# Kernel optimization log

Hardware: AMD Instinct MI355X
Metric: run time of the kernel (lower is better)

Reference implementation:

```python
import jax, jax.numpy as jnp
import numpy as np

T, B, D, K = 256, 128, 1024, 21
PAD = 0


def setup_inputs() -> dict:
    key = jax.random.key(0)
    k1, k2, k3, k4, k5, k6, k7 = jax.random.split(key, 7)
    lstm_features = jax.random.normal(k1, (T, B, D), dtype=jnp.float32)
    # gold tags: non-pad (1..K-1) for a random prefix, PAD afterwards; mask[0] all on
    tags = jax.random.randint(k2, (T, B), 1, K)
    lengths = jax.random.randint(k3, (B,), T // 2, T + 1)
    tags = jnp.where(jnp.arange(T)[:, None] < lengths[None, :], tags, PAD)
    W = jax.random.normal(k4, (D, K), dtype=jnp.float32) * 0.02
    b = jnp.zeros((K,), dtype=jnp.float32)
    # torchcrf initializes transitions uniform(-0.1, 0.1)
    start_transitions = jax.random.uniform(k5, (K,), minval=-0.1, maxval=0.1)
    end_transitions = jax.random.uniform(k6, (K,), minval=-0.1, maxval=0.1)
    transitions = jax.random.uniform(k7, (K, K), minval=-0.1, maxval=0.1)
    return {
        'lstm_features': lstm_features,
        'tags': tags,
        'W': W,
        'b': b,
        'start_transitions': start_transitions,
        'end_transitions': end_transitions,
        'transitions': transitions,
    }


def _crf_nll(emissions, tags, mask, start, end, trans):
    # emissions: (T,B,K), tags/mask: (T,B). Returns -sum_b log p(tags|emissions)
    maskf = mask.astype(emissions.dtype)
    # --- numerator: score of gold path (fully vectorized over t) ---
    em_score = jnp.take_along_axis(emissions, tags[:, :, None], axis=2)[:, :, 0]  # (T,B)
    tr_score = trans[tags[:-1], tags[1:]]                                          # (T-1,B)
    num = start[tags[0]] + em_score[0]
    num = num + jnp.sum((tr_score + em_score[1:]) * maskf[1:], axis=0)
    seq_ends = jnp.sum(mask.astype(jnp.int32), axis=0) - 1                         # (B,)
    last_tags = jnp.take_along_axis(tags, seq_ends[None, :], axis=0)[0]
    num = num + end[last_tags]
    # --- denominator: forward algorithm (log partition) via scan ---
    def step(score, xs):  # score: (B,K)
        emit_t, mask_t = xs
        nxt = jax.nn.logsumexp(score[:, :, None] + trans[None, :, :] + emit_t[:, None, :], axis=1)
        return jnp.where(mask_t[:, None], nxt, score), None
    score0 = start[None, :] + emissions[0]
    scoreT, _ = jax.lax.scan(step, score0, (emissions[1:], mask[1:]))
    den = jax.nn.logsumexp(scoreT + end[None, :], axis=1)                          # (B,)
    return -jnp.sum(num - den)


def _viterbi(emissions, mask, start, end, trans):
    # returns best tag sequence (T,B) int32, padded positions set to PAD
    n_tags = emissions.shape[-1]
    ident = jnp.arange(n_tags, dtype=jnp.int32)[None, :]
    def step(score, xs):  # score: (B,K)
        emit_t, mask_t = xs
        cand = score[:, :, None] + trans[None, :, :]          # (B, prev K, next K)
        best_prev = jnp.argmax(cand, axis=1).astype(jnp.int32)  # (B,K)
        nxt = jnp.max(cand, axis=1) + emit_t
        ptr = jnp.where(mask_t[:, None], best_prev, ident)    # identity ptr on padding
        new_score = jnp.where(mask_t[:, None], nxt, score)
        return new_score, ptr
    score0 = start[None, :] + emissions[0]
    scoreT, history = jax.lax.scan(step, score0, (emissions[1:], mask[1:]))  # history: (T-1,B,K)
    last_tag = jnp.argmax(scoreT + end[None, :], axis=1).astype(jnp.int32)   # (B,)
    def back(tag, hist_t):
        prev = jnp.take_along_axis(hist_t, tag[:, None], axis=1)[:, 0]
        return prev, tag
    first_tag, rest = jax.lax.scan(back, last_tag, history, reverse=True)    # rest = tags[1:]
    best = jnp.concatenate([first_tag[None, :], rest], axis=0)               # (T,B)
    return jnp.where(mask, best, PAD)


def reference(lstm_features, tags, W, b, start_transitions, end_transitions, transitions):
    # Linear projection; dropout is identity at inference
    fc_out = jnp.einsum('tbd,dk->tbk', lstm_features, W) + b
    mask = tags != PAD
    crf_out = _viterbi(fc_out, mask, start_transitions, end_transitions, transitions)
    crf_loss = _crf_nll(fc_out, tags, mask, start_transitions, end_transitions, transitions)
    return crf_out, crf_loss
```

## Files before the change

kernel.cpp:

```cpp
#include <hip/hip_runtime.h>
#include <math.h>

#define T_ 256
#define B_ 128
#define D_ 1024
#define K_ 21
#define NB3 43

typedef short v8s __attribute__((ext_vector_type(8)));
typedef float v4f __attribute__((ext_vector_type(4)));

__device__ __forceinline__ short bf16rne(float f) {
  unsigned u = __float_as_uint(f);
  u += 0x7FFFu + ((u >> 16) & 1u);
  return (short)(u >> 16);
}
__device__ __forceinline__ float rdl(float v, int l) {
  return __int_as_float(__builtin_amdgcn_readlane(__float_as_int(v), l));
}
__device__ __forceinline__ int imax3(int a, int b, int c) {
  const int t = a > b ? a : b;
  return t > c ? t : c;
}

typedef const __attribute__((address_space(1))) void* gas1_t;
typedef __attribute__((address_space(3))) void* las3_t;
__device__ __forceinline__ void gload_lds(const float* g, float* l) {
  __builtin_amdgcn_global_load_lds((gas1_t)g, (las3_t)l, 4, 0, 0);
}

__global__ __launch_bounds__(256) void fc_kernel(
    const float* __restrict__ A, const float* __restrict__ W,
    const float* __restrict__ bias, float* __restrict__ fc,
    float* __restrict__ out_loss) {
  __shared__ float red[3][64][22];
  if (blockIdx.x == 0 && threadIdx.x == 0) *out_loss = 0.f;
  const int lane = threadIdx.x & 63;
  const int wv = threadIdx.x >> 6;
  const int m15 = lane & 15, g4 = lane >> 4;
  const int rowbase = blockIdx.x * 64;
  const int kc = wv * 256;
  const int n1 = 16 + m15;

  v8s bf[8][2];
#pragma unroll
  for (int s = 0; s < 8; ++s) {
    const float* Wp = W + (size_t)(kc + 32 * s + 8 * g4) * K_;
#pragma unroll
    for (int j = 0; j < 8; ++j) bf[s][0][j] = bf16rne(Wp[j * K_ + m15]);
    if (n1 < K_) {
#pragma unroll
      for (int j = 0; j < 8; ++j) bf[s][1][j] = bf16rne(Wp[j * K_ + n1]);
    } else {
#pragma unroll
      for (int j = 0; j < 8; ++j) bf[s][1][j] = 0;
    }
  }

  v4f acc[4][2];
#pragma unroll
  for (int m = 0; m < 4; ++m) {
    acc[m][0] = (v4f)(0.f);
    acc[m][1] = (v4f)(0.f);
  }

#pragma unroll
  for (int s = 0; s < 8; ++s) {
    v8s av[4];
#pragma unroll
    for (int m = 0; m < 4; ++m) {
      const float* Ap =
          A + (size_t)(rowbase + 16 * m + m15) * D_ + kc + 32 * s + 8 * g4;
      const float4 x = *(const float4*)Ap;
      const float4 y = *(const float4*)(Ap + 4);
      av[m][0] = bf16rne(x.x); av[m][1] = bf16rne(x.y);
      av[m][2] = bf16rne(x.z); av[m][3] = bf16rne(x.w);
      av[m][4] = bf16rne(y.x); av[m][5] = bf16rne(y.y);
      av[m][6] = bf16rne(y.z); av[m][7] = bf16rne(y.w);
    }
#pragma unroll
    for (int m = 0; m < 4; ++m) {
      acc[m][0] = __builtin_amdgcn_mfma_f32_16x16x32_bf16(av[m], bf[s][0],
                                                          acc[m][0], 0, 0, 0);
      acc[m][1] = __builtin_amdgcn_mfma_f32_16x16x32_bf16(av[m], bf[s][1],
                                                          acc[m][1], 0, 0, 0);
    }
  }

  if (wv > 0) {
#pragma unroll
    for (int m = 0; m < 4; ++m)
#pragma unroll
      for (int ri = 0; ri < 4; ++ri) {
        const int rl = 16 * m + 4 * g4 + ri;
        red[wv - 1][rl][m15] = acc[m][0][ri];
        if (n1 < K_) red[wv - 1][rl][n1] = acc[m][1][ri];
      }
  }
  __syncthreads();
  if (wv == 0) {
    const float b0 = bias[m15];
    const float b1 = (n1 < K_) ? bias[n1] : 0.f;
#pragma unroll
    for (int m = 0; m < 4; ++m)
#pragma unroll
      for (int ri = 0; ri < 4; ++ri) {
        const int rl = 16 * m + 4 * g4 + ri;
        float* o = fc + (size_t)(rowbase + rl) * K_;
        o[m15] = acc[m][0][ri] + red[0][rl][m15] + red[1][rl][m15] +
                 red[2][rl][m15] + b0;
        if (n1 < K_)
          o[n1] = acc[m][1][ri] + red[0][rl][n1] + red[1][rl][n1] +
                  red[2][rl][n1] + b1;
      }
  }
}

__global__ __launch_bounds__(64) void scan_kernel(
    const float* __restrict__ fc, const int* __restrict__ tags,
    const float* __restrict__ startT, const float* __restrict__ endT,
    const float* __restrict__ trans, float* __restrict__ out_tags,
    float* __restrict__ out_loss) {
  __shared__ v4f statev[18];
  __shared__ float fcs[2][32][64];
  __shared__ unsigned short bp[256 * 66];
  __shared__ unsigned char h2[127 * 66];
  __shared__ unsigned char h4[63 * 66];
  __shared__ unsigned char cur[3 * 256];

  const int lane = threadIdx.x;
  const int blk = blockIdx.x;

  if (blk < 2 * NB3) {
    const bool fwd = blk < NB3;
    const int bblk = fwd ? blk : blk - NB3;
    int g = lane / 21;
    if (g > 2) g = 2;
    int jloc = lane - g * 21;
    if (jloc > 20) jloc = 20;
    const int gj = g * 21 + jloc;
    const int b0 = bblk * 3;

    int len0 = 0, len1 = 0, len2 = 0;
#pragma unroll
    for (int q = 0; q < 4; ++q) {
      const int t = q * 64 + lane;
      int bb0 = b0, bb1 = b0 + 1, bb2 = b0 + 2;
      if (bb1 >= B_) bb1 = B_ - 1;
      if (bb2 >= B_) bb2 = B_ - 1;
      len0 += __popcll(__ballot(tags[t * B_ + bb0] != 0));
      len1 += __popcll(__ballot(tags[t * B_ + bb1] != 0));
      len2 += __popcll(__ballot(tags[t * B_ + bb2] != 0));
    }
    const int mylen = (g == 0) ? len0 : (g == 1) ? len1 : len2;

    float* sb = (float*)statev + g * 24;
    const v4f* sv = (const v4f*)sb;

#define STAGE(c)                                                             \
    {                                                                        \
      const float* src_ = fc + ((size_t)((c) * 32) * B_ + b0) * K_ + lane;   \
      float* dst_ = &fcs[(c) & 1][0][0];                                     \
      _Pragma("unroll")                                                      \
      for (int q_ = 0; q_ < 32; ++q_)                                        \
        gload_lds(src_ + (size_t)q_ * (B_ * K_), dst_ + q_ * 64);            \
    }
#define WAIT_VM0()                                                           \
    {                                                                        \
      asm volatile("s_waitcnt vmcnt(0)" ::: "memory");                       \
      __builtin_amdgcn_sched_barrier(0);                                     \
    }

    STAGE(0)
    WAIT_VM0()
    const float em0 = fcs[0][0][gj];
    STAGE(1)

    if (fwd) {
      float ec[21];
#pragma unroll
      for (int i = 0; i < K_; ++i) ec[i] = __expf(trans[i * K_ + jloc]);
      float p = __expf(startT[jloc] + em0);
      sb[jloc] = p;
      float L = 0.f;

      for (int c = 0; c < 8; ++c) {
        const float* fb = &fcs[c & 1][0][0];
        const int t1 = c * 32 + 32;
        for (int t = c ? c * 32 : 1; t < t1; ++t) {
          const float emt = fb[(t & 31) * 64 + gj];
          const v4f A0 = sv[0], A1 = sv[1], A2 = sv[2], A3 = sv[3],
                    A4 = sv[4];
          const float A5 = sb[20];

          float d0 = A0[0] * ec[0], d1 = A0[1] * ec[1], d2 = A0[2] * ec[2];
          d0 = fmaf(A0[3], ec[3], d0); d1 = fmaf(A1[0], ec[4], d1);
          d2 = fmaf(A1[1], ec[5], d2);
          d0 = fmaf(A1[2], ec[6], d0); d1 = fmaf(A1[3], ec[7], d1);
          d2 = fmaf(A2[0], ec[8], d2);
          d0 = fmaf(A2[1], ec[9], d0); d1 = fmaf(A2[2], ec[10], d1);
          d2 = fmaf(A2[3], ec[11], d2);
          d0 = fmaf(A3[0], ec[12], d0); d1 = fmaf(A3[1], ec[13], d1);
          d2 = fmaf(A3[2], ec[14], d2);
          d0 = fmaf(A3[3], ec[15], d0); d1 = fmaf(A4[0], ec[16], d1);
          d2 = fmaf(A4[1], ec[17], d2);
          d0 = fmaf(A4[2], ec[18], d0); d1 = fmaf(A4[3], ec[19], d1);
          d2 = fmaf(A5, ec[20], d2);

          const float pn = ((d0 + d1) + d2) * __expf(emt);
          p = (t < mylen) ? pn : p;
          if ((t & 7) == 0) {
            const float f = A0[0];
            p *= __builtin_amdgcn_rcpf(f);
            L += __logf(f);
          }
          sb[jloc] = p;
        }
        if (c < 7) {
          WAIT_VM0()
          if (c + 2 < 8) STAGE(c + 2)
        }
      }

      const float w = p * __expf(endT[jloc]);
      float res = 0.f;
#pragma unroll
      for (int gg = 0; gg < 3; ++gg) {
        if (b0 + gg < B_) {
          float tot = 0.f;
#pragma unroll
          for (int i = 0; i < K_; ++i) tot += rdl(w, gg * K_ + i);
          res += rdl(L, gg * K_) + __logf(tot);
        }
      }
      if (lane == 0) atomicAdd(out_loss, res);
    } else {
      float tr[21];
#pragma unroll
      for (int i = 0; i < K_; ++i) tr[i] = trans[i * K_ + jloc] + 2048.0f;
      float sc = startT[jloc] + em0;
      sb[jloc] = sc;

      for (int c = 0; c < 8; ++c) {
        const float* fb = &fcs[c & 1][0][0];
        const int t1 = c * 32 + 32;
        for (int t = c ? c * 32 : 1; t < t1; ++t) {
          const float emt = fb[(t & 31) * 64 + gj];
          const v4f A0 = sv[0], A1 = sv[1], A2 = sv[2], A3 = sv[3],
                    A4 = sv[4];
          const float A5 = sb[20];

#define KEY(i, V) ((__float_as_int((V) + tr[i]) & 0xFFFFFFE0) | (20 - (i)))
          const int q0 = imax3(KEY(0, A0[0]), KEY(1, A0[1]), KEY(2, A0[2]));
          const int q1 = imax3(KEY(3, A0[3]), KEY(4, A1[0]), KEY(5, A1[1]));
          const int q2 = imax3(KEY(6, A1[2]), KEY(7, A1[3]), KEY(8, A2[0]));
          const int q3 = imax3(KEY(9, A2[1]), KEY(10, A2[2]), KEY(11, A2[3]));
          const int q4 = imax3(KEY(12, A3[0]), KEY(13, A3[1]), KEY(14, A3[2]));
          const int q5 = imax3(KEY(15, A3[3]), KEY(16, A4[0]), KEY(17, A4[1]));
          const int q6 = imax3(KEY(18, A4[2]), KEY(19, A4[3]), KEY(20, A5));
          const int km = imax3(imax3(q0, q1, q2), imax3(q3, q4, q5), q6);
#undef KEY
          const float nxt = __int_as_float(km & 0xFFFFFFE0) - 2048.0f + emt;
          const bool m = t < mylen;
          sc = m ? nxt : sc;
          sb[jloc] = sc;
          const int pw = m ? (20 - (km & 31)) : jloc;
          bp[t * 66 + g * 22 + jloc] = (unsigned short)pw;
        }
        if (c < 7) {
          WAIT_VM0()
          if (c + 2 < 8) STAGE(c + 2)
        }
      }
      __syncthreads();

      const float finb = sc + endT[jloc] + 2048.0f;
      const int myk = (__float_as_int(finb) & 0xFFFFFFE0) | (20 - jloc);
      int last0 = 0, last1 = 0, last2 = 0;
#pragma unroll
      for (int gg = 0; gg < 3; ++gg) {
        int km = 0;
#pragma unroll
        for (int i = 0; i < K_; ++i) {
          const int ki = __builtin_amdgcn_readlane(myk, gg * K_ + i);
          km = km > ki ? km : ki;
        }
        const int lt = 20 - (km & 31);
        if (gg == 0) last0 = lt;
        else if (gg == 1) last1 = lt;
        else last2 = lt;
      }

      for (int i = lane; i < 127 * 63; i += 64) {
        const int v = i / 63;
        const int rem = i - v * 63;
        const int gg = rem / 21, j = rem - (rem / 21) * 21;
        h2[v * 66 + gg * 22 + j] = (unsigned char)
            bp[(2 * v + 1) * 66 + gg * 22 + bp[(2 * v + 2) * 66 + gg * 22 + j]];
      }
      __syncthreads();
      for (int i = lane; i < 63 * 63; i += 64) {
        const int w = i / 63;
        const int rem = i - w * 63;
        const int gg = rem / 21, j = rem - (rem / 21) * 21;
        h4[w * 66 + gg * 22 + j] =
            h2[(2 * w) * 66 + gg * 22 + h2[(2 * w + 1) * 66 + gg * 22 + j]];
      }
      __syncthreads();

      if (lane < 3 && b0 + lane < B_) {
        int c = (lane == 0) ? last0 : (lane == 1) ? last1 : last2;
        cur[lane * 256 + 255] = (unsigned char)c;
        c = bp[255 * 66 + lane * 22 + c];
        cur[lane * 256 + 254] = (unsigned char)c;
        c = h2[126 * 66 + lane * 22 + c];
        cur[lane * 256 + 252] = (unsigned char)c;
        for (int w = 62; w >= 0; --w) {
          c = h4[w * 66 + lane * 22 + c];
          cur[lane * 256 + 4 * w] = (unsigned char)c;
        }
      }
      __syncthreads();
      for (int i = lane; i < 63 * 3; i += 64) {
        const int gg = i / 63, ii = i - (i / 63) * 63;
        const int t = 2 + 4 * ii;
        cur[gg * 256 + t] =
            h2[(t >> 1) * 66 + gg * 22 + cur[gg * 256 + t + 2]];
      }
      __syncthreads();
      for (int i = lane; i < 127 * 3; i += 64) {
        const int gg = i / 127, ii = i - (i / 127) * 127;
        const int t = 1 + 2 * ii;
        cur[gg * 256 + t] = (unsigned char)
            bp[(t + 1) * 66 + gg * 22 + cur[gg * 256 + t + 1]];
      }
      __syncthreads();
      for (int i = lane; i < 3 * 256; i += 64) {
        const int gg = i >> 8, t = i & 255;
        const int bb = b0 + gg;
        const int lg = (gg == 0) ? len0 : (gg == 1) ? len1 : len2;
        if (bb < B_)
          out_tags[t * B_ + bb] = (t < lg) ? (float)cur[gg * 256 + t] : 0.f;
      }
    }
#undef STAGE
#undef WAIT_VM0
  } else {
    const int b = blk - 2 * NB3;
    float contrib = 0.f;
#pragma unroll
    for (int q = 0; q < 4; ++q) {
      const int t = lane * 4 + q;
      const int tg = tags[t * B_ + b];
      const size_t ro = ((size_t)t * B_ + b) * K_;
      if (t == 0) {
        contrib += startT[tg] + fc[ro + tg];
      } else if (tg != 0) {
        const int pg = tags[(t - 1) * B_ + b];
        contrib += trans[pg * K_ + tg] + fc[ro + tg];
      }
      const bool isLast =
          (tg != 0) && (t == T_ - 1 || tags[(t + 1) * B_ + b] == 0);
      if (isLast) contrib += endT[tg];
    }
#pragma unroll
    for (int off = 32; off > 0; off >>= 1)
      contrib += __shfl_down(contrib, off, 64);
    if (lane == 0) atomicAdd(out_loss, -contrib);
  }
}

extern "C" void kernel_launch(void* const* d_in, const int* in_sizes, int n_in,
                              void* d_out, int out_size, void* d_ws,
                              size_t ws_size, hipStream_t stream) {
  const float* A = (const float*)d_in[0];
  const int* tags = (const int*)d_in[1];
  const float* W = (const float*)d_in[2];
  const float* bias = (const float*)d_in[3];
  const float* startT = (const float*)d_in[4];
  const float* endT = (const float*)d_in[5];
  const float* trans = (const float*)d_in[6];

  float* out_tags = (float*)d_out;
  float* out_loss = (float*)d_out + (size_t)T_ * B_;
  float* fc = (float*)d_ws;

  fc_kernel<<<512, 256, 0, stream>>>(A, W, bias, fc, out_loss);
  scan_kernel<<<2 * NB3 + B_, 64, 0, stream>>>(fc, tags, startT, endT, trans,
                                               out_tags, out_loss);
}
```

Before: 280.8 us.

## Process six sequences per scan block with two interleaved recurrence chains

Each forward/Viterbi scan block now handles six batch sequences instead of three. Every lane carries two independent recurrence chains (A and B) whose LDS loads and arithmetic are interleaved, so the work per step can overlap the latency of the serial dependency. This halves the number of scan blocks and doubles the LDS footprint and the backtracking work per block. Because the scan was already spread over many mostly idle CUs, the benefit depends on whether the extra instruction-level parallelism outweighs the longer per-step compute on the critical path.

```diff
diff --git a/kernel.cpp b/kernel.cpp
--- a/kernel.cpp
+++ b/kernel.cpp
@@ -5,7 +5,7 @@
 #define B_ 128
 #define D_ 1024
 #define K_ 21
-#define NB3 43
+#define NB6 22
 
 typedef short v8s __attribute__((ext_vector_type(8)));
 typedef float v4f __attribute__((ext_vector_type(4)));
@@ -121,49 +121,59 @@
     const float* __restrict__ startT, const float* __restrict__ endT,
     const float* __restrict__ trans, float* __restrict__ out_tags,
     float* __restrict__ out_loss) {
-  __shared__ v4f statev[18];
-  __shared__ float fcs[2][32][64];
-  __shared__ unsigned short bp[256 * 66];
-  __shared__ unsigned char h2[127 * 66];
-  __shared__ unsigned char h4[63 * 66];
-  __shared__ unsigned char cur[3 * 256];
+  __shared__ v4f statev[36];
+  __shared__ float fcs[2][32][128];
+  __shared__ unsigned short bp[256 * 132];
+  __shared__ unsigned char h2[127 * 132];
+  __shared__ unsigned char h4[63 * 132];
+  __shared__ unsigned char cur[6 * 256];
 
   const int lane = threadIdx.x;
   const int blk = blockIdx.x;
 
-  if (blk < 2 * NB3) {
-    const bool fwd = blk < NB3;
-    const int bblk = fwd ? blk : blk - NB3;
+  if (blk < 2 * NB6) {
+    const bool fwd = blk < NB6;
+    const int bblk = fwd ? blk : blk - NB6;
     int g = lane / 21;
     if (g > 2) g = 2;
     int jloc = lane - g * 21;
     if (jloc > 20) jloc = 20;
-    const int gj = g * 21 + jloc;
-    const int b0 = bblk * 3;
-
-    int len0 = 0, len1 = 0, len2 = 0;
+    const int gjA = g * 21 + jloc;
+    const int gjB = gjA + 63;
+    const int b0 = bblk * 6;
+
+    int len[6];
+#pragma unroll
+    for (int k = 0; k < 6; ++k) len[k] = 0;
 #pragma unroll
     for (int q = 0; q < 4; ++q) {
       const int t = q * 64 + lane;
-      int bb0 = b0, bb1 = b0 + 1, bb2 = b0 + 2;
-      if (bb1 >= B_) bb1 = B_ - 1;
-      if (bb2 >= B_) bb2 = B_ - 1;
-      len0 += __popcll(__ballot(tags[t * B_ + bb0] != 0));
-      len1 += __popcll(__ballot(tags[t * B_ + bb1] != 0));
-      len2 += __popcll(__ballot(tags[t * B_ + bb2] != 0));
-    }
-    const int mylen = (g == 0) ? len0 : (g == 1) ? len1 : len2;
-
-    float* sb = (float*)statev + g * 24;
-    const v4f* sv = (const v4f*)sb;
+#pragma unroll
+      for (int k = 0; k < 6; ++k) {
+        int bb = b0 + k;
+        if (bb >= B_) bb = B_ - 1;
+        len[k] += __popcll(__ballot(tags[t * B_ + bb] != 0));
+      }
+    }
+    const int len0 = len[0], len1 = len[1], len2 = len[2];
+    const int len3 = len[3], len4 = len[4], len5 = len[5];
+    const int mylenA = (g == 0) ? len0 : (g == 1) ? len1 : len2;
+    const int mylenB = (g == 0) ? len3 : (g == 1) ? len4 : len5;
+
+    float* sbA = (float*)statev + g * 24;
+    float* sbB = (float*)statev + (3 + g) * 24;
+    const v4f* svA = (const v4f*)sbA;
+    const v4f* svB = (const v4f*)sbB;
 
 #define STAGE(c)                                                             \
     {                                                                        \
       const float* src_ = fc + ((size_t)((c) * 32) * B_ + b0) * K_ + lane;   \
       float* dst_ = &fcs[(c) & 1][0][0];                                     \
       _Pragma("unroll")                                                      \
-      for (int q_ = 0; q_ < 32; ++q_)                                        \
-        gload_lds(src_ + (size_t)q_ * (B_ * K_), dst_ + q_ * 64);            \
+      for (int q_ = 0; q_ < 32; ++q_) {                                      \
+        gload_lds(src_ + (size_t)q_ * (B_ * K_), dst_ + q_ * 128);           \
+        gload_lds(src_ + (size_t)q_ * (B_ * K_) + 64, dst_ + q_ * 128 + 64); \
+      }                                                                      \
     }
 #define WAIT_VM0()                                                           \
     {                                                                        \
@@ -173,48 +183,75 @@
 
     STAGE(0)
     WAIT_VM0()
-    const float em0 = fcs[0][0][gj];
+    const float em0A = fcs[0][0][gjA];
+    const float em0B = fcs[0][0][gjB];
     STAGE(1)
+
+    const float st0 = startT[jloc];
 
     if (fwd) {
       float ec[21];
 #pragma unroll
       for (int i = 0; i < K_; ++i) ec[i] = __expf(trans[i * K_ + jloc]);
-      float p = __expf(startT[jloc] + em0);
-      sb[jloc] = p;
-      float L = 0.f;
+      float pA = __expf(st0 + em0A), pB = __expf(st0 + em0B);
+      float LA = 0.f, LB = 0.f;
+      sbA[jloc] = pA;
+      sbB[jloc] = pB;
 
       for (int c = 0; c < 8; ++c) {
         const float* fb = &fcs[c & 1][0][0];
         const int t1 = c * 32 + 32;
         for (int t = c ? c * 32 : 1; t < t1; ++t) {
-          const float emt = fb[(t & 31) * 64 + gj];
-          const v4f A0 = sv[0], A1 = sv[1], A2 = sv[2], A3 = sv[3],
-                    A4 = sv[4];
-          const float A5 = sb[20];
-
-          float d0 = A0[0] * ec[0], d1 = A0[1] * ec[1], d2 = A0[2] * ec[2];
-          d0 = fmaf(A0[3], ec[3], d0); d1 = fmaf(A1[0], ec[4], d1);
-          d2 = fmaf(A1[1], ec[5], d2);
-          d0 = fmaf(A1[2], ec[6], d0); d1 = fmaf(A1[3], ec[7], d1);
-          d2 = fmaf(A2[0], ec[8], d2);
-          d0 = fmaf(A2[1], ec[9], d0); d1 = fmaf(A2[2], ec[10], d1);
-          d2 = fmaf(A2[3], ec[11], d2);
-          d0 = fmaf(A3[0], ec[12], d0); d1 = fmaf(A3[1], ec[13], d1);
-          d2 = fmaf(A3[2], ec[14], d2);
-          d0 = fmaf(A3[3], ec[15], d0); d1 = fmaf(A4[0], ec[16], d1);
-          d2 = fmaf(A4[1], ec[17], d2);
-          d0 = fmaf(A4[2], ec[18], d0); d1 = fmaf(A4[3], ec[19], d1);
-          d2 = fmaf(A5, ec[20], d2);
-
-          const float pn = ((d0 + d1) + d2) * __expf(emt);
-          p = (t < mylen) ? pn : p;
+          const float emtA = fb[(t & 31) * 128 + gjA];
+          const float emtB = fb[(t & 31) * 128 + gjB];
+          const v4f A0 = svA[0], A1 = svA[1], A2 = svA[2], A3 = svA[3],
+                    A4 = svA[4];
+          const float A5 = sbA[20];
+          const v4f B0 = svB[0], B1 = svB[1], B2 = svB[2], B3 = svB[3],
+                    B4 = svB[4];
+          const float B5 = sbB[20];
+
+          float a0 = A0[0] * ec[0], a1 = A0[1] * ec[1], a2 = A0[2] * ec[2];
+          a0 = fmaf(A0[3], ec[3], a0); a1 = fmaf(A1[0], ec[4], a1);
+          a2 = fmaf(A1[1], ec[5], a2);
+          a0 = fmaf(A1[2], ec[6], a0); a1 = fmaf(A1[3], ec[7], a1);
+          a2 = fmaf(A2[0], ec[8], a2);
+          a0 = fmaf(A2[1], ec[9], a0); a1 = fmaf(A2[2], ec[10], a1);
+          a2 = fmaf(A2[3], ec[11], a2);
+          a0 = fmaf(A3[0], ec[12], a0); a1 = fmaf(A3[1], ec[13], a1);
+          a2 = fmaf(A3[2], ec[14], a2);
+          a0 = fmaf(A3[3], ec[15], a0); a1 = fmaf(A4[0], ec[16], a1);
+          a2 = fmaf(A4[1], ec[17], a2);
+          a0 = fmaf(A4[2], ec[18], a0); a1 = fmaf(A4[3], ec[19], a1);
+          a2 = fmaf(A5, ec[20], a2);
+          const float pnA = ((a0 + a1) + a2) * __expf(emtA);
+
+          float b0_ = B0[0] * ec[0], b1_ = B0[1] * ec[1], b2_ = B0[2] * ec[2];
+          b0_ = fmaf(B0[3], ec[3], b0_); b1_ = fmaf(B1[0], ec[4], b1_);
+          b2_ = fmaf(B1[1], ec[5], b2_);
+          b0_ = fmaf(B1[2], ec[6], b0_); b1_ = fmaf(B1[3], ec[7], b1_);
+          b2_ = fmaf(B2[0], ec[8], b2_);
+          b0_ = fmaf(B2[1], ec[9], b0_); b1_ = fmaf(B2[2], ec[10], b1_);
+          b2_ = fmaf(B2[3], ec[11], b2_);
+          b0_ = fmaf(B3[0], ec[12], b0_); b1_ = fmaf(B3[1], ec[13], b1_);
+          b2_ = fmaf(B3[2], ec[14], b2_);
+          b0_ = fmaf(B3[3], ec[15], b0_); b1_ = fmaf(B4[0], ec[16], b1_);
+          b2_ = fmaf(B4[1], ec[17], b2_);
+          b0_ = fmaf(B4[2], ec[18], b0_); b1_ = fmaf(B4[3], ec[19], b1_);
+          b2_ = fmaf(B5, ec[20], b2_);
+          const float pnB = ((b0_ + b1_) + b2_) * __expf(emtB);
+
+          pA = (t < mylenA) ? pnA : pA;
+          pB = (t < mylenB) ? pnB : pB;
           if ((t & 7) == 0) {
-            const float f = A0[0];
-            p *= __builtin_amdgcn_rcpf(f);
-            L += __logf(f);
+            const float fA = A0[0], fB = B0[0];
+            pA *= __builtin_amdgcn_rcpf(fA);
+            LA += __logf(fA);
+            pB *= __builtin_amdgcn_rcpf(fB);
+            LB += __logf(fB);
           }
-          sb[jloc] = p;
+          sbA[jloc] = pA;
+          sbB[jloc] = pB;
         }
         if (c < 7) {
           WAIT_VM0()
@@ -222,15 +259,23 @@
         }
       }
 
-      const float w = p * __expf(endT[jloc]);
+      const float eT = __expf(endT[jloc]);
+      const float wA = pA * eT, wB = pB * eT;
       float res = 0.f;
 #pragma unroll
-      for (int gg = 0; gg < 3; ++gg) {
+      for (int gg = 0; gg < 6; ++gg) {
         if (b0 + gg < B_) {
+          const int base = (gg % 3) * 21;
           float tot = 0.f;
-#pragma unroll
-          for (int i = 0; i < K_; ++i) tot += rdl(w, gg * K_ + i);
-          res += rdl(L, gg * K_) + __logf(tot);
+          if (gg < 3) {
+#pragma unroll
+            for (int i = 0; i < K_; ++i) tot += rdl(wA, base + i);
+            res += rdl(LA, base) + __logf(tot);
+          } else {
+#pragma unroll
+            for (int i = 0; i < K_; ++i) tot += rdl(wB, base + i);
+            res += rdl(LB, base) + __logf(tot);
+          }
         }
       }
       if (lane == 0) atomicAdd(out_loss, res);
@@ -238,34 +283,56 @@
       float tr[21];
 #pragma unroll
       for (int i = 0; i < K_; ++i) tr[i] = trans[i * K_ + jloc] + 2048.0f;
-      float sc = startT[jloc] + em0;
-      sb[jloc] = sc;
+      float scA = st0 + em0A, scB = st0 + em0B;
+      sbA[jloc] = scA;
+      sbB[jloc] = scB;
 
       for (int c = 0; c < 8; ++c) {
         const float* fb = &fcs[c & 1][0][0];
         const int t1 = c * 32 + 32;
         for (int t = c ? c * 32 : 1; t < t1; ++t) {
-          const float emt = fb[(t & 31) * 64 + gj];
-          const v4f A0 = sv[0], A1 = sv[1], A2 = sv[2], A3 = sv[3],
-                    A4 = sv[4];
-          const float A5 = sb[20];
+          const float emtA = fb[(t & 31) * 128 + gjA];
+          const float emtB = fb[(t & 31) * 128 + gjB];
+          const v4f A0 = svA[0], A1 = svA[1], A2 = svA[2], A3 = svA[3],
+                    A4 = svA[4];
+          const float A5 = sbA[20];
+          const v4f B0 = svB[0], B1 = svB[1], B2 = svB[2], B3 = svB[3],
+                    B4 = svB[4];
+          const float B5 = sbB[20];
 
 #define KEY(i, V) ((__float_as_int((V) + tr[i]) & 0xFFFFFFE0) | (20 - (i)))
-          const int q0 = imax3(KEY(0, A0[0]), KEY(1, A0[1]), KEY(2, A0[2]));
-          const int q1 = imax3(KEY(3, A0[3]), KEY(4, A1[0]), KEY(5, A1[1]));
-          const int q2 = imax3(KEY(6, A1[2]), KEY(7, A1[3]), KEY(8, A2[0]));
-          const int q3 = imax3(KEY(9, A2[1]), KEY(10, A2[2]), KEY(11, A2[3]));
-          const int q4 = imax3(KEY(12, A3[0]), KEY(13, A3[1]), KEY(14, A3[2]));
-          const int q5 = imax3(KEY(15, A3[3]), KEY(16, A4[0]), KEY(17, A4[1]));
-          const int q6 = imax3(KEY(18, A4[2]), KEY(19, A4[3]), KEY(20, A5));
-          const int km = imax3(imax3(q0, q1, q2), imax3(q3, q4, q5), q6);
+          const int qa0 = imax3(KEY(0, A0[0]), KEY(1, A0[1]), KEY(2, A0[2]));
+          const int qa1 = imax3(KEY(3, A0[3]), KEY(4, A1[0]), KEY(5, A1[1]));
+          const int qa2 = imax3(KEY(6, A1[2]), KEY(7, A1[3]), KEY(8, A2[0]));
+          const int qa3 = imax3(KEY(9, A2[1]), KEY(10, A2[2]), KEY(11, A2[3]));
+          const int qa4 = imax3(KEY(12, A3[0]), KEY(13, A3[1]), KEY(14, A3[2]));
+          const int qa5 = imax3(KEY(15, A3[3]), KEY(16, A4[0]), KEY(17, A4[1]));
+          const int qa6 = imax3(KEY(18, A4[2]), KEY(19, A4[3]), KEY(20, A5));
+          const int kmA = imax3(imax3(qa0, qa1, qa2), imax3(qa3, qa4, qa5),
+                                qa6);
+          const int qb0 = imax3(KEY(0, B0[0]), KEY(1, B0[1]), KEY(2, B0[2]));
+          const int qb1 = imax3(KEY(3, B0[3]), KEY(4, B1[0]), KEY(5, B1[1]));
+          const int qb2 = imax3(KEY(6, B1[2]), KEY(7, B1[3]), KEY(8, B2[0]));
+          const int qb3 = imax3(KEY(9, B2[1]), KEY(10, B2[2]), KEY(11, B2[3]));
+          const int qb4 = imax3(KEY(12, B3[0]), KEY(13, B3[1]), KEY(14, B3[2]));
+          const int qb5 = imax3(KEY(15, B3[3]), KEY(16, B4[0]), KEY(17, B4[1]));
+          const int qb6 = imax3(KEY(18, B4[2]), KEY(19, B4[3]), KEY(20, B5));
+          const int kmB = imax3(imax3(qb0, qb1, qb2), imax3(qb3, qb4, qb5),
+                                qb6);
 #undef KEY
-          const float nxt = __int_as_float(km & 0xFFFFFFE0) - 2048.0f + emt;
-          const bool m = t < mylen;
-          sc = m ? nxt : sc;
-          sb[jloc] = sc;
-          const int pw = m ? (20 - (km & 31)) : jloc;
-          bp[t * 66 + g * 22 + jloc] = (unsigned short)pw;
+          const float nxtA =
+              __int_as_float(kmA & 0xFFFFFFE0) - 2048.0f + emtA;
+          const float nxtB =
+              __int_as_float(kmB & 0xFFFFFFE0) - 2048.0f + emtB;
+          const bool mA = t < mylenA, mB = t < mylenB;
+          scA = mA ? nxtA : scA;
+          scB = mB ? nxtB : scB;
+          sbA[jloc] = scA;
+          sbB[jloc] = scB;
+          const int pwA = mA ? (20 - (kmA & 31)) : jloc;
+          const int pwB = mB ? (20 - (kmB & 31)) : jloc;
+          bp[t * 132 + g * 22 + jloc] = (unsigned short)pwA;
+          bp[t * 132 + (3 + g) * 22 + jloc] = (unsigned short)pwB;
         }
         if (c < 7) {
           WAIT_VM0()
@@ -274,71 +341,79 @@
       }
       __syncthreads();
 
-      const float finb = sc + endT[jloc] + 2048.0f;
-      const int myk = (__float_as_int(finb) & 0xFFFFFFE0) | (20 - jloc);
-      int last0 = 0, last1 = 0, last2 = 0;
-#pragma unroll
-      for (int gg = 0; gg < 3; ++gg) {
+      const float eTl = endT[jloc] + 2048.0f;
+      const int mykA = (__float_as_int(scA + eTl) & 0xFFFFFFE0) | (20 - jloc);
+      const int mykB = (__float_as_int(scB + eTl) & 0xFFFFFFE0) | (20 - jloc);
+      int last[6];
+#pragma unroll
+      for (int gg = 0; gg < 6; ++gg) {
+        const int base = (gg % 3) * 21;
         int km = 0;
 #pragma unroll
         for (int i = 0; i < K_; ++i) {
-          const int ki = __builtin_amdgcn_readlane(myk, gg * K_ + i);
+          const int ki = __builtin_amdgcn_readlane(gg < 3 ? mykA : mykB,
+                                                   base + i);
           km = km > ki ? km : ki;
         }
-        const int lt = 20 - (km & 31);
-        if (gg == 0) last0 = lt;
-        else if (gg == 1) last1 = lt;
-        else last2 = lt;
-      }
-
-      for (int i = lane; i < 127 * 63; i += 64) {
-        const int v = i / 63;
-        const int rem = i - v * 63;
+        last[gg] = 20 - (km & 31);
+      }
+      const int last0 = last[0], last1 = last[1], last2 = last[2];
+      const int last3 = last[3], last4 = last[4], last5 = last[5];
+
+      for (int i = lane; i < 127 * 126; i += 64) {
+        const int v = i / 126;
+        const int rem = i - v * 126;
         const int gg = rem / 21, j = rem - (rem / 21) * 21;
-        h2[v * 66 + gg * 22 + j] = (unsigned char)
-            bp[(2 * v + 1) * 66 + gg * 22 + bp[(2 * v + 2) * 66 + gg * 22 + j]];
-      }
-      __syncthreads();
-      for (int i = lane; i < 63 * 63; i += 64) {
-        const int w = i / 63;
-        const int rem = i - w * 63;
+        h2[v * 132 + gg * 22 + j] = (unsigned char)
+            bp[(2 * v + 1) * 132 + gg * 22 +
+               bp[(2 * v + 2) * 132 + gg * 22 + j]];
+      }
+      __syncthreads();
+      for (int i = lane; i < 63 * 126; i += 64) {
+        const int w2 = i / 126;
+        const int rem = i - w2 * 126;
         const int gg = rem / 21, j = rem - (rem / 21) * 21;
-        h4[w * 66 + gg * 22 + j] =
-            h2[(2 * w) * 66 + gg * 22 + h2[(2 * w + 1) * 66 + gg * 22 + j]];
-      }
-      __syncthreads();
-
-      if (lane < 3 && b0 + lane < B_) {
-        int c = (lane == 0) ? last0 : (lane == 1) ? last1 : last2;
+        h4[w2 * 132 + gg * 22 + j] =
+            h2[(2 * w2) * 132 + gg * 22 +
+               h2[(2 * w2 + 1) * 132 + gg * 22 + j]];
+      }
+      __syncthreads();
+
+      if (lane < 6 && b0 + lane < B_) {
+        int c = (lane == 0) ? last0 : (lane == 1) ? last1
+                : (lane == 2) ? last2 : (lane == 3) ? last3
+                : (lane == 4) ? last4 : last5;
         cur[lane * 256 + 255] = (unsigned char)c;
-        c = bp[255 * 66 + lane * 22 + c];
+        c = bp[255 * 132 + lane * 22 + c];
         cur[lane * 256 + 254] = (unsigned char)c;
-        c = h2[126 * 66 + lane * 22 + c];
+        c = h2[126 * 132 + lane * 22 + c];
         cur[lane * 256 + 252] = (unsigned char)c;
-        for (int w = 62; w >= 0; --w) {
-          c = h4[w * 66 + lane * 22 + c];
-          cur[lane * 256 + 4 * w] = (unsigned char)c;
-        }
-      }
-      __syncthreads();
-      for (int i = lane; i < 63 * 3; i += 64) {
+        for (int w2 = 62; w2 >= 0; --w2) {
+          c = h4[w2 * 132 + lane * 22 + c];
+          cur[lane * 256 + 4 * w2] = (unsigned char)c;
+        }
+      }
+      __syncthreads();
+      for (int i = lane; i < 63 * 6; i += 64) {
         const int gg = i / 63, ii = i - (i / 63) * 63;
         const int t = 2 + 4 * ii;
         cur[gg * 256 + t] =
-            h2[(t >> 1) * 66 + gg * 22 + cur[gg * 256 + t + 2]];
-      }
-      __syncthreads();
-      for (int i = lane; i < 127 * 3; i += 64) {
+            h2[(t >> 1) * 132 + gg * 22 + cur[gg * 256 + t + 2]];
+      }
+      __syncthreads();
+      for (int i = lane; i < 127 * 6; i += 64) {
         const int gg = i / 127, ii = i - (i / 127) * 127;
         const int t = 1 + 2 * ii;
         cur[gg * 256 + t] = (unsigned char)
-            bp[(t + 1) * 66 + gg * 22 + cur[gg * 256 + t + 1]];
-      }
-      __syncthreads();
-      for (int i = lane; i < 3 * 256; i += 64) {
+            bp[(t + 1) * 132 + gg * 22 + cur[gg * 256 + t + 1]];
+      }
+      __syncthreads();
+      for (int i = lane; i < 6 * 256; i += 64) {
         const int gg = i >> 8, t = i & 255;
         const int bb = b0 + gg;
-        const int lg = (gg == 0) ? len0 : (gg == 1) ? len1 : len2;
+        const int lg = (gg == 0) ? len0 : (gg == 1) ? len1
+                      : (gg == 2) ? len2 : (gg == 3) ? len3
+                      : (gg == 4) ? len4 : len5;
         if (bb < B_)
           out_tags[t * B_ + bb] = (t < lg) ? (float)cur[gg * 256 + t] : 0.f;
       }
@@ -346,7 +421,7 @@
 #undef STAGE
 #undef WAIT_VM0
   } else {
-    const int b = blk - 2 * NB3;
+    const int b = blk - 2 * NB6;
     float contrib = 0.f;
 #pragma unroll
     for (int q = 0; q < 4; ++q) {
@@ -386,6 +461,6 @@
   float* fc = (float*)d_ws;
 
   fc_kernel<<<512, 256, 0, stream>>>(A, W, bias, fc, out_loss);
-  scan_kernel<<<2 * NB3 + B_, 64, 0, stream>>>(fc, tags, startT, endT, trans,
+  scan_kernel<<<2 * NB6 + B_, 64, 0, stream>>>(fc, tags, startT, endT, trans,
                                                out_tags, out_loss);
 }
```

Result: slower. 338.1 us (+20.4%).
